# Kernel tuning notes

Hardware: AMD Instinct MI355X
Metric: run time of the kernel (lower is better)

Reference implementation:

```python
import jax, jax.numpy as jnp
import numpy as np

N_NODES = 100000


def gcn_conv(x, edge_index, W, b, n_nodes):
    # PyG GCNConv: h = x @ W; add self-loops; symmetric normalization; aggregate to dst; + bias
    h = x @ W  # [N, out]
    loop = jnp.arange(n_nodes, dtype=edge_index.dtype)
    src = jnp.concatenate([edge_index[0], loop])
    dst = jnp.concatenate([edge_index[1], loop])
    ones = jnp.ones(src.shape[0], dtype=h.dtype)
    deg = jax.ops.segment_sum(ones, dst, num_segments=n_nodes)  # in-degree incl. self-loop
    dinv = jnp.where(deg > 0, jax.lax.rsqrt(deg), 0.0)
    norm = dinv[src] * dinv[dst]  # [E+N]
    msgs = h[src] * norm[:, None]  # gather + scale
    out = jax.ops.segment_sum(msgs, dst, num_segments=n_nodes)  # scatter-add
    return out + b


def setup_inputs() -> dict:
    key = jax.random.key(0)
    k1, k2, k3, k4 = jax.random.split(key, 4)
    x = jax.random.normal(k1, (N_NODES, 256), dtype=jnp.float32)
    edge_index = jax.random.randint(k2, (2, 3200000), 0, N_NODES, dtype=jnp.int64)
    W1 = jax.random.normal(k3, (256, 64), dtype=jnp.float32) * (1.0 / np.sqrt(256))
    b1 = jnp.zeros((64,), dtype=jnp.float32)
    W2 = jax.random.normal(k4, (64, 40), dtype=jnp.float32) * (1.0 / np.sqrt(64))
    b2 = jnp.zeros((40,), dtype=jnp.float32)
    return {"x": x, "edge_index": edge_index, "W1": W1, "b1": b1, "W2": W2, "b2": b2}


def reference(x, edge_index, W1, b1, W2, b2):
    n = x.shape[0]
    h = gcn_conv(x, edge_index, W1, b1, n)
    h = jax.nn.relu(h)
    h = gcn_conv(h, edge_index, W2, b2, n)
    return jax.nn.log_softmax(h, axis=1)
```

## Files before the change

kernel.cpp:

```cpp
#include <hip/hip_runtime.h>
#include <hip/hip_bf16.h>
#include <math.h>

static constexpr int NN    = 100000;
static constexpr int BSH   = 9;
static constexpr int NBUCK = (NN + 511) >> 9;
static constexpr int EPB   = 8192;
static constexpr int SCT   = 1024;
static constexpr int CAP   = 24576;

typedef __attribute__((ext_vector_type(8))) short short8;
typedef __attribute__((ext_vector_type(4))) float f32x4;
typedef __attribute__((ext_vector_type(2))) float f32x2;

#if defined(__has_builtin)
#  if __has_builtin(__builtin_amdgcn_cvt_pk_f32_fp8) && __has_builtin(__builtin_amdgcn_cvt_pk_fp8_f32)
#    define USE_HW_FP8 1
#  endif
#endif
#ifndef USE_HW_FP8
#  define USE_HW_FP8 0
#endif

__device__ __forceinline__ short f2bf(float f) {
    __hip_bfloat16 h = __float2bfloat16(f);
    return __builtin_bit_cast(short, h);
}

__device__ __forceinline__ float fp8_dec_sw(unsigned b) {
    unsigned u = ((b & 0x80u) << 24) | ((b & 0x7Fu) << 20);
    return __builtin_bit_cast(float, u) * 0x1p120f;
}
__device__ __forceinline__ unsigned fp8_enc_sw(float f) {
    unsigned u = __builtin_bit_cast(unsigned, f * 0x1p-120f);
    unsigned s = (u >> 24) & 0x80u;
    unsigned mag = u & 0x7FFFFFFFu;
    unsigned t = mag + 0x7FFFFu + ((mag >> 20) & 1u);
    unsigned r = t >> 20;
    if (r > 0x7Eu) r = 0x7Eu;
    return s | r;
}

template<bool HI>
__device__ __forceinline__ f32x2 dec2w(unsigned u) {
#if USE_HW_FP8
    return __builtin_amdgcn_cvt_pk_f32_fp8(u, HI);
#else
    unsigned w = HI ? (u >> 16) : u;
    f32x2 r;
    r.x = fp8_dec_sw(w & 0xFFu);
    r.y = fp8_dec_sw((w >> 8) & 0xFFu);
    return r;
#endif
}
__device__ __forceinline__ unsigned enc2(float a, float b) {
#if USE_HW_FP8
    return (unsigned)__builtin_amdgcn_cvt_pk_fp8_f32(a, b, 0, false);
#else
    return fp8_enc_sw(a) | (fp8_enc_sw(b) << 8);
#endif
}

__device__ __forceinline__ void acc8(f32x2* a, uint2 u) {
    a[0] += dec2w<false>(u.x);
    a[1] += dec2w<true>(u.x);
    a[2] += dec2w<false>(u.y);
    a[3] += dec2w<true>(u.y);
}

__device__ __forceinline__ long long ldidx(const void* __restrict__ p, long long i, int is64) {
    if (is64) return ((const long long* __restrict__)p)[i];
    return (long long)((const int* __restrict__)p)[i];
}

template<int K, int NCOLS, int KT, int NT>
__device__ __forceinline__ void packB_dev(const float* __restrict__ W,
                                          short* __restrict__ P, int t) {
    if (t >= KT * NT * 64) return;
    int kt = t / (NT * 64);
    int nt = (t / 64) % NT;
    int l  = t & 63;
    int g  = l >> 4;
#pragma unroll
    for (int e = 0; e < 8; ++e) {
        int k   = kt * 32 + g * 8 + e;
        int col = nt * 16 + (l & 15);
        float v = (col < NCOLS) ? W[k * NCOLS + col] : 0.0f;
        P[t * 8 + e] = f2bf(v);
    }
}

__global__ void __launch_bounds__(256)
k_init(const unsigned int* __restrict__ e32, int* __restrict__ flag,
       int* __restrict__ gcur,
       const float* __restrict__ W1, short* __restrict__ pB1,
       const float* __restrict__ W2, short* __restrict__ pB2) {
    int blk = blockIdx.x, tid = threadIdx.x;
    if (blk == 0) {
        if (tid < NBUCK) gcur[tid] = 0;
        __shared__ int any_nz;
        if (tid == 0) any_nz = 0;
        __syncthreads();
        unsigned int nz = 0;
        for (int w = 1 + 2 * tid; w < 4096; w += 512)
            nz |= e32[w];
        if (nz) atomicOr(&any_nz, 1);
        __syncthreads();
        if (tid == 0) *flag = (any_nz == 0) ? 1 : 0;
    } else if (blk <= 8) {
        packB_dev<256, 64, 8, 4>(W1, pB1, (blk - 1) * 256 + tid);
    } else {
        packB_dev<64, 40, 2, 3>(W2, pB2, (blk - 9) * 256 + tid);
    }
}

__global__ void __launch_bounds__(SCT)
k_scatter_bucket(const void* __restrict__ eidx, const int* __restrict__ flag, long long E,
                 int* __restrict__ gcur, unsigned* __restrict__ ebuf) {
    __shared__ int h[NBUCK];
    for (int b = threadIdx.x; b < NBUCK; b += SCT) h[b] = 0;
    __syncthreads();
    int is64 = *flag;
    long long base = (long long)blockIdx.x * EPB;
    long long end  = base + EPB < E ? base + EPB : E;
    unsigned sv[8], dv[8];
    bool ok[8];
#pragma unroll
    for (int k = 0; k < 8; ++k) {
        long long e = base + (long long)k * SCT + threadIdx.x;
        ok[k] = (e < end);
        if (ok[k]) {
            sv[k] = (unsigned)ldidx(eidx, e, is64);
            dv[k] = (unsigned)ldidx(eidx, E + e, is64);
            atomicAdd(&h[dv[k] >> BSH], 1);
        }
    }
    __syncthreads();
    for (int b = threadIdx.x; b < NBUCK; b += SCT)
        h[b] = atomicAdd(&gcur[b], h[b]);
    __syncthreads();
#pragma unroll
    for (int k = 0; k < 8; ++k) {
        if (ok[k]) {
            int bk = dv[k] >> BSH;
            int pos = atomicAdd(&h[bk], 1);
            ebuf[(long long)bk * CAP + pos] = sv[k] | ((dv[k] & 511u) << 17);
        }
    }
}

__global__ void k_bucket_starts(const int* __restrict__ gcnt, int* __restrict__ bstart,
                                int* __restrict__ rowst, int n) {
    if (threadIdx.x == 0) {
        int run = 0;
        for (int b = 0; b < NBUCK; ++b) { bstart[b] = run; run += gcnt[b]; }
        bstart[NBUCK] = run;
        rowst[n] = run;
    }
}

__global__ void __launch_bounds__(1024)
k_bucket_csr(const unsigned* __restrict__ ebuf, const int* __restrict__ gcnt,
             const int* __restrict__ bstart, int* __restrict__ rowst,
             float* __restrict__ dinv, int* __restrict__ csr) {
    __shared__ int cnt[512];
    __shared__ int cursor[512];
    __shared__ int woff[8];
    int b = blockIdx.x;
    int t = threadIdx.x;
    int cb = gcnt[b];
    long long rbase = (long long)b * CAP;
    int bs = bstart[b];
    if (t < 512) cnt[t] = 0;
    __syncthreads();
    for (int i = t; i < cb; i += 1024) {
        unsigned ed = ebuf[rbase + i];
        atomicAdd(&cnt[ed >> 17], 1);
    }
    __syncthreads();
    int v = 0, ps = 0;
    if (t < 512) {
        v = cnt[t];
        ps = v;
        int lane = t & 63;
#pragma unroll
        for (int off = 1; off < 64; off <<= 1) {
            int up = __shfl_up(ps, off);
            if (lane >= off) ps += up;
        }
        if (lane == 63) woff[t >> 6] = ps;
    }
    __syncthreads();
    if (t == 0) {
        int run = 0;
#pragma unroll
        for (int i = 0; i < 8; ++i) { int x = woff[i]; woff[i] = run; run += x; }
    }
    __syncthreads();
    if (t < 512) {
        int incl  = ps + woff[t >> 6];
        int start = bs + incl - v;
        int gnode = (b << BSH) + t;
        if (gnode < NN) {
            rowst[gnode] = start;
            dinv[gnode]  = rsqrtf((float)(v + 1));
        }
        cursor[t] = start;
    }
    __syncthreads();
    for (int i = t; i < cb; i += 1024) {
        unsigned ed = ebuf[rbase + i];
        int pos = atomicAdd(&cursor[ed >> 17], 1);
        csr[pos] = (int)(ed & 0x1FFFFu);
    }
}

template<int K, int NCOLS, int KT, int NT, bool ABF16>
__global__ void __launch_bounds__(256)
k_mfma_gemm(const void* __restrict__ Xv, const short* __restrict__ packedB,
            const float* __restrict__ dinv, unsigned char* __restrict__ H, int n) {
    __shared__ alignas(16) short sW[KT * NT * 512];
    short8* dst = (short8*)sW;
    const short8* src = (const short8*)packedB;
    constexpr int TOT8 = KT * NT * 64;
    for (int i = threadIdx.x; i < TOT8; i += 256) dst[i] = src[i];
    __syncthreads();

    int wave = threadIdx.x >> 6, lane = threadIdx.x & 63;
    int g = lane >> 4;
    int arow = blockIdx.x * 64 + wave * 16 + (lane & 15);

    f32x4 acc[NT];
#pragma unroll
    for (int nt = 0; nt < NT; ++nt) acc[nt] = (f32x4){0.f, 0.f, 0.f, 0.f};

#pragma unroll
    for (int kt = 0; kt < KT; ++kt) {
        short8 a;
        if (arow < n) {
            int k0 = kt * 32 + g * 8;
            if (ABF16) {
                const short* xr = (const short*)Xv + (long long)arow * K;
                a = *(const short8*)(xr + k0);
            } else {
                const float* xr = (const float*)Xv + (long long)arow * K;
                float4 u = *(const float4*)(xr + k0);
                float4 v = *(const float4*)(xr + k0 + 4);
                a[0] = f2bf(u.x); a[1] = f2bf(u.y); a[2] = f2bf(u.z); a[3] = f2bf(u.w);
                a[4] = f2bf(v.x); a[5] = f2bf(v.y); a[6] = f2bf(v.z); a[7] = f2bf(v.w);
            }
        } else {
            a = (short8){0, 0, 0, 0, 0, 0, 0, 0};
        }
#pragma unroll
        for (int nt = 0; nt < NT; ++nt) {
            short8 bfr = dst[(kt * NT + nt) * 64 + lane];
            acc[nt] = __builtin_amdgcn_mfma_f32_16x16x32_bf16(a, bfr, acc[nt], 0, 0, 0);
        }
    }

    int c = lane & 15;
    int orow_base = blockIdx.x * 64 + wave * 16 + g * 4;
#pragma unroll
    for (int r = 0; r < 4; ++r) {
        int orow = orow_base + r;
        if (orow < n) {
            float di = dinv[orow];
            float v[NT];
#pragma unroll
            for (int nt = 0; nt < NT; ++nt) v[nt] = acc[nt][r] * di;
            unsigned char* hp = H + (long long)orow * NCOLS;
#pragma unroll
            for (int p = 0; p < NT; p += 2) {
                unsigned wrd = enc2(v[p], (p + 1 < NT) ? v[p + 1] : 0.0f);
                int col0 = p * 16 + c;
                if (col0 < NCOLS) hp[col0] = (unsigned char)(wrd & 0xFFu);
                if (p + 1 < NT) {
                    int col1 = col0 + 16;
                    if (col1 < NCOLS) hp[col1] = (unsigned char)((wrd >> 8) & 0xFFu);
                }
            }
        }
    }
}

__global__ void __launch_bounds__(256)
k_gather_relu(const int* __restrict__ rowst, const int* __restrict__ csr,
              const unsigned char* __restrict__ h1s, const float* __restrict__ dinv,
              const float* __restrict__ b, unsigned short* __restrict__ out, int n) {
    long long gid = (long long)blockIdx.x * blockDim.x + threadIdx.x;
    int node = (int)(gid >> 3);
    int fe   = (int)(gid & 7);
    if (node >= n) return;
    int jb = rowst[node], je = rowst[node + 1];
    unsigned feoff = (unsigned)fe << 3;

    f32x2 a0[4], a1[4];
#pragma unroll
    for (int q = 0; q < 4; ++q) { a0[q] = (f32x2){0.f, 0.f}; a1[q] = (f32x2){0.f, 0.f}; }

    int j = jb;
    for (; j + 1 < je; j += 2) {
        int s0 = csr[j];
        int s1 = csr[j + 1];
        uint2 u0 = *(const uint2*)(h1s + (((unsigned)s0 << 6) + feoff));
        uint2 u1 = *(const uint2*)(h1s + (((unsigned)s1 << 6) + feoff));
        acc8(a0, u0);
        acc8(a1, u1);
    }
    if (j < je) {
        int s0 = csr[j];
        uint2 u0 = *(const uint2*)(h1s + (((unsigned)s0 << 6) + feoff));
        acc8(a0, u0);
    }
#pragma unroll
    for (int q = 0; q < 4; ++q) a0[q] += a1[q];

    uint2 self = *(const uint2*)(h1s + (((unsigned)node << 6) + feoff));
    acc8(a0, self);
    float di = dinv[node];
    unsigned short r[8];
#pragma unroll
    for (int q = 0; q < 4; ++q) {
        float v0 = fmaxf(a0[q].x * di + b[8 * fe + 2 * q],     0.0f);
        float v1 = fmaxf(a0[q].y * di + b[8 * fe + 2 * q + 1], 0.0f);
        r[2 * q]     = (unsigned short)f2bf(v0);
        r[2 * q + 1] = (unsigned short)f2bf(v1);
    }
    uint4 pk;
    pk.x = (unsigned)r[0] | ((unsigned)r[1] << 16);
    pk.y = (unsigned)r[2] | ((unsigned)r[3] << 16);
    pk.z = (unsigned)r[4] | ((unsigned)r[5] << 16);
    pk.w = (unsigned)r[6] | ((unsigned)r[7] << 16);
    ((uint4*)(out + (long long)node * 64))[fe] = pk;
}

__global__ void __launch_bounds__(256)
k_gather_lsm(const int* __restrict__ rowst, const int* __restrict__ csr,
             const unsigned char* __restrict__ h2s, const float* __restrict__ dinv,
             const float* __restrict__ b, float* __restrict__ out, int n) {
    long long gid = (long long)blockIdx.x * blockDim.x + threadIdx.x;
    int node = (int)(gid >> 3);
    int fe   = (int)(gid & 7);
    if (node >= n) return;
    bool act = (fe < 5);
    int jb = rowst[node], je = rowst[node + 1];
    unsigned feoff = (unsigned)fe << 3;

    f32x2 a0[4], a1[4];
#pragma unroll
    for (int q = 0; q < 4; ++q) { a0[q] = (f32x2){0.f, 0.f}; a1[q] = (f32x2){0.f, 0.f}; }

    int j = jb;
    for (; j + 1 < je; j += 2) {
        int s0 = csr[j];
        int s1 = csr[j + 1];
        if (act) {
            uint2 u0 = *(const uint2*)(h2s + ((unsigned)s0 * 40u + feoff));
            uint2 u1 = *(const uint2*)(h2s + ((unsigned)s1 * 40u + feoff));
            acc8(a0, u0);
            acc8(a1, u1);
        }
    }
    if (j < je && act) {
        int s0 = csr[j];
        uint2 u0 = *(const uint2*)(h2s + ((unsigned)s0 * 40u + feoff));
        acc8(a0, u0);
    }
#pragma unroll
    for (int q = 0; q < 4; ++q) a0[q] += a1[q];

    float va[8];
    float mloc = -INFINITY;
    if (act) {
        uint2 self = *(const uint2*)(h2s + ((unsigned)node * 40u + feoff));
        acc8(a0, self);
        float di = dinv[node];
#pragma unroll
        for (int q = 0; q < 4; ++q) {
            va[2 * q]     = a0[q].x * di + b[8 * fe + 2 * q];
            va[2 * q + 1] = a0[q].y * di + b[8 * fe + 2 * q + 1];
            mloc = fmaxf(mloc, fmaxf(va[2 * q], va[2 * q + 1]));
        }
    }
    float m = mloc;
    m = fmaxf(m, __shfl_xor(m, 1));
    m = fmaxf(m, __shfl_xor(m, 2));
    m = fmaxf(m, __shfl_xor(m, 4));
    float ex = 0.0f;
    if (act) {
#pragma unroll
        for (int k = 0; k < 8; ++k) ex += __expf(va[k] - m);
    }
    ex += __shfl_xor(ex, 1);
    ex += __shfl_xor(ex, 2);
    ex += __shfl_xor(ex, 4);
    float lse = __logf(ex);
    if (act) {
        float4 r0 = make_float4(va[0] - m - lse, va[1] - m - lse,
                                va[2] - m - lse, va[3] - m - lse);
        float4 r1 = make_float4(va[4] - m - lse, va[5] - m - lse,
                                va[6] - m - lse, va[7] - m - lse);
        *(float4*)(out + (long long)node * 40 + 8 * fe)     = r0;
        *(float4*)(out + (long long)node * 40 + 8 * fe + 4) = r1;
    }
}

extern "C" void kernel_launch(void* const* d_in, const int* in_sizes, int n_in,
                              void* d_out, int out_size, void* d_ws, size_t ws_size,
                              hipStream_t stream) {
    const float* x  = (const float*)d_in[0];
    const void*  ei = d_in[1];
    const float* W1 = (const float*)d_in[2];
    const float* b1 = (const float*)d_in[3];
    const float* W2 = (const float*)d_in[4];
    const float* b2 = (const float*)d_in[5];
    float* out = (float*)d_out;

    const long long E = (long long)in_sizes[1] / 2;
    const int nblk = (int)((E + EPB - 1) / EPB);

    char* w = (char*)d_ws;
    auto alloc = [&](size_t bytes) -> void* {
        void* p = (void*)w;
        w += (bytes + 255) & ~(size_t)255;
        return p;
    };
    int*      flag    = (int*)     alloc(4);
    int*      gcur    = (int*)     alloc((size_t)NBUCK * 4);
    int*      bstart  = (int*)     alloc(((size_t)NBUCK + 1) * 4);
    int*      rowst   = (int*)     alloc(((size_t)NN + 1) * 4);
    float*    dinv    = (float*)   alloc((size_t)NN * 4);
    short*    pB1     = (short*)   alloc((size_t)8 * 4 * 64 * 8 * 2);
    short*    pB2     = (short*)   alloc((size_t)2 * 3 * 64 * 8 * 2);
    int*      csr     = (int*)     alloc((size_t)E * 4);
    unsigned* ebuf    = (unsigned*)alloc((size_t)NBUCK * CAP * 4);
    unsigned short* agg1 = (unsigned short*)alloc((size_t)NN * 64 * 2);
    unsigned char* h1s = (unsigned char*)ebuf;
    unsigned char* h2s = h1s;

    const int B = 256;
    auto cdiv = [](long long a, long long b) { return (int)((a + b - 1) / b); };

    k_init<<<11, B, 0, stream>>>((const unsigned int*)ei, flag, gcur, W1, pB1, W2, pB2);

    k_scatter_bucket<<<nblk, SCT, 0, stream>>>(ei, flag, E, gcur, ebuf);
    k_bucket_starts<<<1, 64, 0, stream>>>(gcur, bstart, rowst, NN);
    k_bucket_csr<<<NBUCK, 1024, 0, stream>>>(ebuf, gcur, bstart, rowst, dinv, csr);

    k_mfma_gemm<256, 64, 8, 4, false><<<cdiv(NN, 64), B, 0, stream>>>(x, pB1, dinv, h1s, NN);

    k_gather_relu<<<cdiv((long long)NN * 8, B), B, 0, stream>>>(rowst, csr, h1s, dinv, b1, agg1, NN);

    k_mfma_gemm<64, 40, 2, 3, true><<<cdiv(NN, 64), B, 0, stream>>>(agg1, pB2, dinv, h2s, NN);

    k_gather_lsm<<<cdiv((long long)NN * 8, B), B, 0, stream>>>(rowst, csr, h2s, dinv, b2, out, NN);
}
```

Measured before the change: 193.4 us.

## Fuse edge bucketing with first GEMM and fold source-degree scaling into gather

Merges the edge scatter-bucket pass and the layer-1 MFMA GEMM into one launch. Blocks below nsblk do the bucketing and the rest compute x@W1, so the memory-bound scatter and the compute-bound GEMM can overlap. Since the GEMM now runs before dinv exists, the source-side normalisation moves into the layer-1 gather, which loads dinv[src] per edge and applies it with an FMA. The separate bucket-starts kernel is dropped; each CSR block sums the preceding bucket counts with shared atomics. h1s gets its own buffer instead of aliasing ebuf, which costs extra workspace and adds a random dinv load per edge.

After: 192.9 us. No clear change (-0.3%).

```diff
diff --git a/kernel.cpp b/kernel.cpp
--- a/kernel.cpp
+++ b/kernel.cpp
@@ -6,7 +6,6 @@
 static constexpr int BSH   = 9;
 static constexpr int NBUCK = (NN + 511) >> 9;
 static constexpr int EPB   = 8192;
-static constexpr int SCT   = 1024;
 static constexpr int CAP   = 24576;
 
 typedef __attribute__((ext_vector_type(8))) short short8;
@@ -66,6 +65,13 @@
     a[1] += dec2w<true>(u.x);
     a[2] += dec2w<false>(u.y);
     a[3] += dec2w<true>(u.y);
+}
+__device__ __forceinline__ void acc8s(f32x2* a, uint2 u, float ds) {
+    f32x2 w = {ds, ds};
+    a[0] = dec2w<false>(u.x) * w + a[0];
+    a[1] = dec2w<true>(u.x)  * w + a[1];
+    a[2] = dec2w<false>(u.y) * w + a[2];
+    a[3] = dec2w<true>(u.y)  * w + a[3];
 }
 
 __device__ __forceinline__ long long ldidx(const void* __restrict__ p, long long i, int is64) {
@@ -114,70 +120,120 @@
     }
 }
 
-__global__ void __launch_bounds__(SCT)
-k_scatter_bucket(const void* __restrict__ eidx, const int* __restrict__ flag, long long E,
-                 int* __restrict__ gcur, unsigned* __restrict__ ebuf) {
-    __shared__ int h[NBUCK];
-    for (int b = threadIdx.x; b < NBUCK; b += SCT) h[b] = 0;
-    __syncthreads();
-    int is64 = *flag;
-    long long base = (long long)blockIdx.x * EPB;
-    long long end  = base + EPB < E ? base + EPB : E;
-    unsigned sv[8], dv[8];
-    bool ok[8];
-#pragma unroll
-    for (int k = 0; k < 8; ++k) {
-        long long e = base + (long long)k * SCT + threadIdx.x;
-        ok[k] = (e < end);
-        if (ok[k]) {
-            sv[k] = (unsigned)ldidx(eidx, e, is64);
-            dv[k] = (unsigned)ldidx(eidx, E + e, is64);
-            atomicAdd(&h[dv[k] >> BSH], 1);
-        }
-    }
-    __syncthreads();
-    for (int b = threadIdx.x; b < NBUCK; b += SCT)
-        h[b] = atomicAdd(&gcur[b], h[b]);
-    __syncthreads();
-#pragma unroll
-    for (int k = 0; k < 8; ++k) {
-        if (ok[k]) {
-            int bk = dv[k] >> BSH;
-            int pos = atomicAdd(&h[bk], 1);
-            ebuf[(long long)bk * CAP + pos] = sv[k] | ((dv[k] & 511u) << 17);
-        }
-    }
-}
-
-__global__ void k_bucket_starts(const int* __restrict__ gcnt, int* __restrict__ bstart,
-                                int* __restrict__ rowst, int n) {
-    if (threadIdx.x == 0) {
-        int run = 0;
-        for (int b = 0; b < NBUCK; ++b) { bstart[b] = run; run += gcnt[b]; }
-        bstart[NBUCK] = run;
-        rowst[n] = run;
+__global__ void __launch_bounds__(1024)
+k_build_gemm1(const void* __restrict__ eidx, const int* __restrict__ flag, long long E,
+              int nsblk, int* __restrict__ gcur, unsigned* __restrict__ ebuf,
+              const float* __restrict__ X, const short* __restrict__ pB1,
+              unsigned char* __restrict__ H, int n) {
+    if ((int)blockIdx.x < nsblk) {
+        __shared__ int h[NBUCK];
+        for (int b = threadIdx.x; b < NBUCK; b += 1024) h[b] = 0;
+        __syncthreads();
+        int is64 = *flag;
+        long long base = (long long)blockIdx.x * EPB;
+        long long end  = base + EPB < E ? base + EPB : E;
+        unsigned sv[8], dv[8];
+        bool ok[8];
+#pragma unroll
+        for (int k = 0; k < 8; ++k) {
+            long long e = base + (long long)k * 1024 + threadIdx.x;
+            ok[k] = (e < end);
+            if (ok[k]) {
+                sv[k] = (unsigned)ldidx(eidx, e, is64);
+                dv[k] = (unsigned)ldidx(eidx, E + e, is64);
+                atomicAdd(&h[dv[k] >> BSH], 1);
+            }
+        }
+        __syncthreads();
+        for (int b = threadIdx.x; b < NBUCK; b += 1024)
+            h[b] = atomicAdd(&gcur[b], h[b]);
+        __syncthreads();
+#pragma unroll
+        for (int k = 0; k < 8; ++k) {
+            if (ok[k]) {
+                int bk = dv[k] >> BSH;
+                int pos = atomicAdd(&h[bk], 1);
+                ebuf[(long long)bk * CAP + pos] = sv[k] | ((dv[k] & 511u) << 17);
+            }
+        }
+    } else {
+        __shared__ alignas(16) short sW[8 * 4 * 512];
+        short8* dst = (short8*)sW;
+        const short8* src = (const short8*)pB1;
+        int tid = threadIdx.x;
+        for (int i = tid; i < 2048; i += 1024) dst[i] = src[i];
+        __syncthreads();
+
+        int gblk = (int)blockIdx.x - nsblk;
+        int wave = tid >> 6, lane = tid & 63;
+        int g = lane >> 4;
+        int arow = gblk * 256 + wave * 16 + (lane & 15);
+
+        f32x4 acc[4];
+#pragma unroll
+        for (int nt = 0; nt < 4; ++nt) acc[nt] = (f32x4){0.f, 0.f, 0.f, 0.f};
+
+#pragma unroll
+        for (int kt = 0; kt < 8; ++kt) {
+            short8 a;
+            if (arow < n) {
+                const float* xr = X + (long long)arow * 256;
+                int k0 = kt * 32 + g * 8;
+                float4 u = *(const float4*)(xr + k0);
+                float4 v = *(const float4*)(xr + k0 + 4);
+                a[0] = f2bf(u.x); a[1] = f2bf(u.y); a[2] = f2bf(u.z); a[3] = f2bf(u.w);
+                a[4] = f2bf(v.x); a[5] = f2bf(v.y); a[6] = f2bf(v.z); a[7] = f2bf(v.w);
+            } else {
+                a = (short8){0, 0, 0, 0, 0, 0, 0, 0};
+            }
+#pragma unroll
+            for (int nt = 0; nt < 4; ++nt) {
+                short8 bfr = dst[(kt * 4 + nt) * 64 + lane];
+                acc[nt] = __builtin_amdgcn_mfma_f32_16x16x32_bf16(a, bfr, acc[nt], 0, 0, 0);
+            }
+        }
+
+        int c = lane & 15;
+        int orow_base = gblk * 256 + wave * 16 + g * 4;
+#pragma unroll
+        for (int r = 0; r < 4; ++r) {
+            int orow = orow_base + r;
+            if (orow < n) {
+                unsigned char* hp = H + (long long)orow * 64;
+#pragma unroll
+                for (int p = 0; p < 4; p += 2) {
+                    unsigned wrd = enc2(acc[p][r], acc[p + 1][r]);
+                    hp[p * 16 + c]        = (unsigned char)(wrd & 0xFFu);
+                    hp[(p + 1) * 16 + c]  = (unsigned char)((wrd >> 8) & 0xFFu);
+                }
+            }
+        }
     }
 }
 
 __global__ void __launch_bounds__(1024)
 k_bucket_csr(const unsigned* __restrict__ ebuf, const int* __restrict__ gcnt,
-             const int* __restrict__ bstart, int* __restrict__ rowst,
-             float* __restrict__ dinv, int* __restrict__ csr) {
+             int* __restrict__ rowst, float* __restrict__ dinv,
+             int* __restrict__ csr, int n) {
     __shared__ int cnt[512];
     __shared__ int cursor[512];
     __shared__ int woff[8];
+    __shared__ int bs_sh;
     int b = blockIdx.x;
     int t = threadIdx.x;
     int cb = gcnt[b];
     long long rbase = (long long)b * CAP;
-    int bs = bstart[b];
+    if (t == 0) bs_sh = 0;
     if (t < 512) cnt[t] = 0;
     __syncthreads();
+    if (t < b) atomicAdd(&bs_sh, gcnt[t]);
     for (int i = t; i < cb; i += 1024) {
         unsigned ed = ebuf[rbase + i];
         atomicAdd(&cnt[ed >> 17], 1);
     }
     __syncthreads();
+    int bs = bs_sh;
+    if (b == NBUCK - 1 && t == 0) rowst[n] = bs + cb;
     int v = 0, ps = 0;
     if (t < 512) {
         v = cnt[t];
@@ -201,7 +257,7 @@
         int incl  = ps + woff[t >> 6];
         int start = bs + incl - v;
         int gnode = (b << BSH) + t;
-        if (gnode < NN) {
+        if (gnode < n) {
             rowst[gnode] = start;
             dinv[gnode]  = rsqrtf((float)(v + 1));
         }
@@ -303,27 +359,30 @@
     for (; j + 1 < je; j += 2) {
         int s0 = csr[j];
         int s1 = csr[j + 1];
+        float ds0 = dinv[s0];
+        float ds1 = dinv[s1];
         uint2 u0 = *(const uint2*)(h1s + (((unsigned)s0 << 6) + feoff));
         uint2 u1 = *(const uint2*)(h1s + (((unsigned)s1 << 6) + feoff));
-        acc8(a0, u0);
-        acc8(a1, u1);
+        acc8s(a0, u0, ds0);
+        acc8s(a1, u1, ds1);
     }
     if (j < je) {
         int s0 = csr[j];
+        float ds0 = dinv[s0];
         uint2 u0 = *(const uint2*)(h1s + (((unsigned)s0 << 6) + feoff));
-        acc8(a0, u0);
+        acc8s(a0, u0, ds0);
     }
 #pragma unroll
     for (int q = 0; q < 4; ++q) a0[q] += a1[q];
 
+    float dn = dinv[node];
     uint2 self = *(const uint2*)(h1s + (((unsigned)node << 6) + feoff));
-    acc8(a0, self);
-    float di = dinv[node];
+    acc8s(a0, self, dn);
     unsigned short r[8];
 #pragma unroll
     for (int q = 0; q < 4; ++q) {
-        float v0 = fmaxf(a0[q].x * di + b[8 * fe + 2 * q],     0.0f);
-        float v1 = fmaxf(a0[q].y * di + b[8 * fe + 2 * q + 1], 0.0f);
+        float v0 = fmaxf(a0[q].x * dn + b[8 * fe + 2 * q],     0.0f);
+        float v1 = fmaxf(a0[q].y * dn + b[8 * fe + 2 * q + 1], 0.0f);
         r[2 * q]     = (unsigned short)f2bf(v0);
         r[2 * q + 1] = (unsigned short)f2bf(v1);
     }
@@ -418,7 +477,8 @@
     float* out = (float*)d_out;
 
     const long long E = (long long)in_sizes[1] / 2;
-    const int nblk = (int)((E + EPB - 1) / EPB);
+    const int nsblk = (int)((E + EPB - 1) / EPB);
+    const int ngblk = (NN + 255) / 256;
 
     char* w = (char*)d_ws;
     auto alloc = [&](size_t bytes) -> void* {
@@ -428,15 +488,14 @@
     };
     int*      flag    = (int*)     alloc(4);
     int*      gcur    = (int*)     alloc((size_t)NBUCK * 4);
-    int*      bstart  = (int*)     alloc(((size_t)NBUCK + 1) * 4);
     int*      rowst   = (int*)     alloc(((size_t)NN + 1) * 4);
     float*    dinv    = (float*)   alloc((size_t)NN * 4);
     short*    pB1     = (short*)   alloc((size_t)8 * 4 * 64 * 8 * 2);
     short*    pB2     = (short*)   alloc((size_t)2 * 3 * 64 * 8 * 2);
     int*      csr     = (int*)     alloc((size_t)E * 4);
     unsigned* ebuf    = (unsigned*)alloc((size_t)NBUCK * CAP * 4);
+    unsigned char* h1s = (unsigned char*)alloc((size_t)NN * 64);
     unsigned short* agg1 = (unsigned short*)alloc((size_t)NN * 64 * 2);
-    unsigned char* h1s = (unsigned char*)ebuf;
     unsigned char* h2s = h1s;
 
     const int B = 256;
@@ -444,11 +503,10 @@
 
     k_init<<<11, B, 0, stream>>>((const unsigned int*)ei, flag, gcur, W1, pB1, W2, pB2);
 
-    k_scatter_bucket<<<nblk, SCT, 0, stream>>>(ei, flag, E, gcur, ebuf);
-    k_bucket_starts<<<1, 64, 0, stream>>>(gcur, bstart, rowst, NN);
-    k_bucket_csr<<<NBUCK, 1024, 0, stream>>>(ebuf, gcur, bstart, rowst, dinv, csr);
-
-    k_mfma_gemm<256, 64, 8, 4, false><<<cdiv(NN, 64), B, 0, stream>>>(x, pB1, dinv, h1s, NN);
+    k_build_gemm1<<<nsblk + ngblk, 1024, 0, stream>>>(ei, flag, E, nsblk, gcur, ebuf,
+                                                      x, pB1, h1s, NN);
+
+    k_bucket_csr<<<NBUCK, 1024, 0, stream>>>(ebuf, gcur, rowst, dinv, csr, NN);
 
     k_gather_relu<<<cdiv((long long)NN * 8, B), B, 0, stream>>>(rowst, csr, h1s, dinv, b1, agg1, NN);
 
```
